# Performance work log

Hardware: AMD Instinct MI355X
Metric: run time of the kernel (lower is better)

The kernel has to match this reference:

```python
import jax, jax.numpy as jnp
import numpy as np

B, T, D = 128, 2048, 4      # batch paths, hedging steps, input features
H, A, W = 64, 32, 10        # hidden_size, attention_dim, memory_length
DMAX = 1.5
SCALE = float(np.sqrt(A))


def setup_inputs() -> dict:
    key = jax.random.key(0)
    ks = jax.random.split(key, 24)

    def rn(k, shape, s=0.1):
        return (jax.random.normal(k, shape) * s).astype(jnp.float32)

    inp = {"x": rn(ks[0], (B, T, D), 1.0)}
    names = [
        ("W_ih0", (4 * H, D)), ("W_hh0", (4 * H, H)), ("b_ih0", (4 * H,)), ("b_hh0", (4 * H,)),
        ("W_ih1", (4 * H, H)), ("W_hh1", (4 * H, H)), ("b_ih1", (4 * H,)), ("b_hh1", (4 * H,)),
        ("Wq", (A, H)), ("bq", (A,)), ("Wk", (A, H)), ("bk", (A,)),
        ("Wv", (H, H)), ("bv", (H,)), ("Wc", (H, 2 * H)), ("bc", (H,)),
        ("Wo1", (H // 2, H)), ("bo1", (H // 2,)), ("Wo2", (1, H // 2)), ("bo2", (1,)),
    ]
    for i, (n, s) in enumerate(names):
        inp[n] = rn(ks[i + 1], s)
    return inp


def _lstm_cell(xt, h, c, Wih, Whh, bih, bhh):
    g = xt @ Wih.T + h @ Whh.T + bih + bhh
    i, f, gg, o = jnp.split(g, 4, axis=-1)  # torch gate order i,f,g,o
    c = jax.nn.sigmoid(f) * c + jax.nn.sigmoid(i) * jnp.tanh(gg)
    h = jax.nn.sigmoid(o) * jnp.tanh(c)
    return h, c


def _forward(x, W_ih0, W_hh0, b_ih0, b_hh0, W_ih1, W_hh1, b_ih1, b_hh1,
             Wq, bq, Wk, bk, Wv, bv, Wc, bc, Wo1, bo1, Wo2, bo2):
    b, t, _ = x.shape
    z = jnp.zeros((b, H), x.dtype)

    def step(carry, xt):
        h0, c0, h1, c1 = carry
        h0, c0 = _lstm_cell(xt, h0, c0, W_ih0, W_hh0, b_ih0, b_hh0)
        h1, c1 = _lstm_cell(h0, h1, c1, W_ih1, W_hh1, b_ih1, b_hh1)
        return (h0, c0, h1, c1), h1

    _, hs = jax.lax.scan(step, (z, z, z, z), jnp.swapaxes(x, 0, 1))  # [T,B,H]
    lstm_out = jnp.swapaxes(hs, 0, 1)  # [B,T,H]

    # sliding-window causal attention over the last W hidden states (strictly past)
    q = lstm_out @ Wq.T + bq          # [B,T,A]
    k = lstm_out @ Wk.T + bk          # [B,T,A]
    v = lstm_out @ Wv.T + bv          # [B,T,H]

    idx = jnp.arange(t)[:, None] - jnp.arange(1, W + 1)[None, :]  # [T,W], t-1..t-W
    mask = idx >= 0
    idxc = jnp.clip(idx, 0, t - 1)
    k_win = k[:, idxc]                # [B,T,W,A]
    v_win = v[:, idxc]                # [B,T,W,H]

    scores = jnp.einsum('bta,btwa->btw', q, k_win) / SCALE
    scores = jnp.where(mask[None], scores, jnp.float32(-1e9))
    weights = jax.nn.softmax(scores, axis=-1)
    context = jnp.einsum('btw,btwh->bth', weights, v_win)  # [B,T,H]

    combined = jnp.concatenate([lstm_out, context], axis=-1) @ Wc.T + bc
    # at t == 0 the original skips attention and uses h_t directly
    combined = jnp.where((jnp.arange(t) == 0)[None, :, None], lstm_out, combined)

    raw = jax.nn.relu(combined @ Wo1.T + bo1) @ Wo2.T + bo2  # [B,T,1]
    return DMAX * jnp.tanh(raw[..., 0])                      # [B,T]


def reference(x, W_ih0, W_hh0, b_ih0, b_hh0, W_ih1, W_hh1, b_ih1, b_hh1,
              Wq, bq, Wk, bk, Wv, bv, Wc, bc, Wo1, bo1, Wo2, bo2):
    return _forward(x, W_ih0, W_hh0, b_ih0, b_hh0, W_ih1, W_hh1, b_ih1, b_hh1,
                    Wq, bq, Wk, bk, Wv, bv, Wc, bc, Wo1, bo1, Wo2, bo2)
```

## Files before the change

### kernel.cpp

```cpp
#include <hip/hip_runtime.h>
#include <hip/hip_bf16.h>
#include <math.h>

#define BB   128
#define TT   2048
#define DD   4
#define HH   64
#define WIN  10
#define TILE 64
#define RWS  (TILE + WIN)

__device__ __forceinline__ float sigf(float x) {
    return __fdividef(1.f, 1.f + __expf(-x));
}
__device__ __forceinline__ float dot4(float4 a, float4 b) {
    return a.x*b.x + a.y*b.y + a.z*b.z + a.w*b.w;
}

#define QB(x, imm) __int_as_float(__builtin_amdgcn_mov_dpp(__float_as_int(x), (imm), 0xF, 0xF, true))
__device__ __forceinline__ float red8(float x) {
    x = x + QB(x, 0xB1);
    x = x + QB(x, 0x4E);
    x = x + QB(x, 0x141);
    return x;
}

__device__ __forceinline__ void act_update(const float gv0, const float gv1,
                                           const float gv2, const float gv3,
                                           const int q, float& c, float& h) {
    float y = gv0;
    y = (q == 1) ? gv1 : y;
    y = (q == 2) ? gv2 : y;
    y = (q == 3) ? gv3 : y;
    y = (q == 2) ? y + y : y;
    float s = sigf(y);
    s = (q == 2) ? s + s - 1.f : s;
    const float ii = QB(s, 0x00);
    const float ff = QB(s, 0x55);
    const float gg = QB(s, 0xAA);
    const float oo = QB(s, 0xFF);
    c = ff * c + ii * gg;
    h = oo * (2.f * sigf(c + c) - 1.f);
}

#define PIN4(v) asm volatile("" : "+v"(v.x), "+v"(v.y), "+v"(v.z), "+v"(v.w))

__global__ __launch_bounds__(512, 1)
void lstm_kernel(const float* __restrict__ x,
                 const float* __restrict__ Wih0, const float* __restrict__ Whh0,
                 const float* __restrict__ bih0, const float* __restrict__ bhh0,
                 const float* __restrict__ Wih1, const float* __restrict__ Whh1,
                 const float* __restrict__ bih1, const float* __restrict__ bhh1,
                 float* __restrict__ lstm_out) {
    __shared__ __align__(16) float h0s[2][HH];
    __shared__ __align__(16) float h1s[2][HH];
    __shared__ __align__(16) float xall[TT * DD];
    __shared__ __align__(16) float hbuf[64 * HH];

    const int tid = threadIdx.x;
    const int u   = tid >> 3;
    const int p   = tid & 7;
    const int q   = tid & 3;
    const int b   = blockIdx.x;

    float4 wh0[4][2], wi1[4][2], wh1[4][2];
    float  wx[4], b0g[4], b1g[4];
#pragma unroll
    for (int g = 0; g < 4; ++g) {
        const int row = g * 64 + u;
        wh0[g][0] = *(const float4*)(Whh0 + row * 64 + 8 * p);
        wh0[g][1] = *(const float4*)(Whh0 + row * 64 + 8 * p + 4);
        wi1[g][0] = *(const float4*)(Wih1 + row * 64 + 8 * p);
        wi1[g][1] = *(const float4*)(Wih1 + row * 64 + 8 * p + 4);
        wh1[g][0] = *(const float4*)(Whh1 + row * 64 + 8 * p);
        wh1[g][1] = *(const float4*)(Whh1 + row * 64 + 8 * p + 4);
        wx[g]  = (p < 4) ? Wih0[row * 4 + p] : 0.f;
        b0g[g] = bih0[row] + bhh0[row];
        b1g[g] = bih1[row] + bhh1[row];
    }
#pragma unroll
    for (int g = 0; g < 4; ++g) {
#pragma unroll
        for (int c = 0; c < 2; ++c) {
            PIN4(wh0[g][c]);
            PIN4(wi1[g][c]);
            PIN4(wh1[g][c]);
        }
        asm volatile("" : "+v"(wx[g]), "+v"(b0g[g]), "+v"(b1g[g]));
    }

    const float* xrow = x + (size_t)b * TT * DD;
    for (int i = tid; i < TT; i += 512)
        *(float4*)(xall + i * 4) = *(const float4*)(xrow + i * 4);
    if (tid < HH) h1s[1][tid] = 0.f;
    float c0 = 0.f, c1 = 0.f;
    __syncthreads();

    {
        const float xa = xall[p & 3];
        float g0v[4];
#pragma unroll
        for (int g = 0; g < 4; ++g) g0v[g] = red8(wx[g] * xa) + b0g[g];
        float h0v;
        act_update(g0v[0], g0v[1], g0v[2], g0v[3], q, c0, h0v);
        if (p == 0) h0s[0][u] = h0v;
    }

    float* orow = lstm_out + (size_t)b * TT * HH;

    for (int t = 0; t < TT; ++t) {
        __syncthreads();
        const float* h0c = h0s[t & 1];
        const float* h1p = h1s[(t + 1) & 1];
        const float4 h0a = *(const float4*)(h0c + 8 * p);
        const float4 h0b = *(const float4*)(h0c + 8 * p + 4);
        const float4 h1a = *(const float4*)(h1p + 8 * p);
        const float4 h1b = *(const float4*)(h1p + 8 * p + 4);

        float g1v[4], g0v[4];
#pragma unroll
        for (int g = 0; g < 4; ++g) {
            const float sA = dot4(wi1[g][0], h0a) + dot4(wh1[g][0], h1a);
            const float sB = dot4(wi1[g][1], h0b) + dot4(wh1[g][1], h1b);
            g1v[g] = sA + sB;
        }
        const float xa = xall[(t + 1 < TT ? t + 1 : t) * 4 + (p & 3)];
#pragma unroll
        for (int g = 0; g < 4; ++g) {
            const float sA = wx[g] * xa + dot4(wh0[g][0], h0a);
            const float sB = dot4(wh0[g][1], h0b);
            g0v[g] = sA + sB;
        }
#pragma unroll
        for (int g = 0; g < 4; ++g) g1v[g] = red8(g1v[g]) + b1g[g];
#pragma unroll
        for (int g = 0; g < 4; ++g) g0v[g] = red8(g0v[g]) + b0g[g];

        {
            float h1vv;
            act_update(g1v[0], g1v[1], g1v[2], g1v[3], q, c1, h1vv);
            if (p == 0) h1s[t & 1][u] = h1vv;
            if (p == 1) hbuf[(t & 63) * HH + u] = h1vv;
        }
        if (t + 1 < TT) {
            float h0vv;
            act_update(g0v[0], g0v[1], g0v[2], g0v[3], q, c0, h0vv);
            if (p == 0) h0s[(t + 1) & 1][u] = h0vv;
        }
        if ((t & 63) == 63) {
            __syncthreads();
            float4*       dst = (float4*)(orow + (size_t)(t - 63) * HH);
            const float4* src = (const float4*)hbuf;
            dst[tid]       = src[tid];
            dst[512 + tid] = src[512 + tid];
        }
    }
}

#define ATTN_LDS_FLOATS 19560

__global__ __launch_bounds__(256, 2)
void attn_kernel(const float* __restrict__ lstm,
                 const float* __restrict__ Wq, const float* __restrict__ bq,
                 const float* __restrict__ Wk, const float* __restrict__ bk,
                 const float* __restrict__ Wv, const float* __restrict__ bv,
                 const float* __restrict__ Wc, const float* __restrict__ bc,
                 const float* __restrict__ Wo1, const float* __restrict__ bo1,
                 const float* __restrict__ Wo2, const float* __restrict__ bo2,
                 float* __restrict__ out) {
    extern __shared__ __align__(16) float lds[];
    float* bias = lds;
    float* ho   = lds + 256;
    float* kb   = lds + 4992;
    float* qb   = lds + 7656;
    float* vb   = lds + 9960;
    float* swr  = lds + 14696;
    float* ctxs = lds + 15464;
    float* cmbs = lds + 4992;
    float* o1s  = lds + 9960;

    const int tid  = threadIdx.x;
    const int b    = blockIdx.x >> 5;
    const int tile = blockIdx.x & 31;
    const int t0   = tile * TILE;

    if (tid < 32) {
        bias[tid]       = bq[tid];
        bias[32 + tid]  = bk[tid];
        bias[192 + tid] = bo1[tid];
        bias[224 + tid] = Wo2[tid];
    }
    if (tid >= 64 && tid < 128) {
        const int j = tid - 64;
        bias[64 + j]  = bv[j];
        bias[128 + j] = bc[j];
    }
    for (int i = tid; i < RWS * 16; i += 256) {
        const int row = i >> 4, c = i & 15;
        const int t = t0 - WIN + row;
        float4 v = make_float4(0.f, 0.f, 0.f, 0.f);
        if (t >= 0) v = *(const float4*)(lstm + ((size_t)b * TT + t) * HH + 4 * c);
        *(float4*)(ho + row * 64 + 4 * c) = v;
    }
    __syncthreads();

    {
        const int h = tid & 63, rq = tid >> 6;
        const int r0 = rq * 19;
        int ri[19];
        float acc[19];
#pragma unroll
        for (int rr = 0; rr < 19; ++rr) { ri[rr] = min(r0 + rr, RWS - 1); acc[rr] = bias[64 + h]; }
#pragma unroll
        for (int k4 = 0; k4 < 16; ++k4) {
            const float4 w = *(const float4*)(Wv + h * 64 + 4 * k4);
#pragma unroll
            for (int rr = 0; rr < 19; ++rr)
                acc[rr] += dot4(w, *(const float4*)(ho + ri[rr] * 64 + 4 * k4));
        }
#pragma unroll
        for (int rr = 0; rr < 19; ++rr) vb[ri[rr] * 64 + h] = acc[rr];
    }
    {
        const int a = tid & 31, rq = tid >> 5;
        const int r0 = rq * 10;
        int ri[10];
        float acc[10];
#pragma unroll
        for (int rr = 0; rr < 10; ++rr) { ri[rr] = min(r0 + rr, RWS - 1); acc[rr] = bias[32 + a]; }
#pragma unroll
        for (int k4 = 0; k4 < 16; ++k4) {
            const float4 w = *(const float4*)(Wk + a * 64 + 4 * k4);
#pragma unroll
            for (int rr = 0; rr < 10; ++rr)
                acc[rr] += dot4(w, *(const float4*)(ho + ri[rr] * 64 + 4 * k4));
        }
#pragma unroll
        for (int rr = 0; rr < 10; ++rr) kb[ri[rr] * 36 + a] = acc[rr];
    }
    {
        const int a = tid & 31, rq = tid >> 5;
        float acc[8];
#pragma unroll
        for (int rr = 0; rr < 8; ++rr) acc[rr] = bias[a];
#pragma unroll
        for (int k4 = 0; k4 < 16; ++k4) {
            const float4 w = *(const float4*)(Wq + a * 64 + 4 * k4);
#pragma unroll
            for (int rr = 0; rr < 8; ++rr)
                acc[rr] += dot4(w, *(const float4*)(ho + (rq * 8 + rr + WIN) * 64 + 4 * k4));
        }
#pragma unroll
        for (int rr = 0; rr < 8; ++rr) qb[(rq * 8 + rr) * 36 + a] = acc[rr];
    }
    __syncthreads();

    for (int i = tid; i < TILE * WIN; i += 256) {
        const int r = i / WIN, l = i - r * WIN;
        const int t = t0 + r;
        float s = -1e30f;
        if (t - 1 - l >= 0) {
            const int kr = r + WIN - 1 - l;
            float acc = 0.f;
#pragma unroll
            for (int a4 = 0; a4 < 8; ++a4)
                acc += dot4(*(const float4*)(qb + r * 36 + 4 * a4),
                            *(const float4*)(kb + kr * 36 + 4 * a4));
            s = acc * 0.17677669529663687f;
        }
        swr[r * 12 + l] = s;
    }
    __syncthreads();
    if (tid < TILE) {
        const int r = tid;
        float sc[WIN], m = -1e30f;
#pragma unroll
        for (int l = 0; l < WIN; ++l) { sc[l] = swr[r * 12 + l]; m = fmaxf(m, sc[l]); }
        float sum = 0.f;
#pragma unroll
        for (int l = 0; l < WIN; ++l) { sc[l] = __expf(sc[l] - m); sum += sc[l]; }
        const float inv = __fdividef(1.f, sum);
#pragma unroll
        for (int l = 0; l < WIN; ++l) swr[r * 12 + l] = sc[l] * inv;
    }
    __syncthreads();
    for (int i = tid; i < TILE * HH; i += 256) {
        const int r = i >> 6, h = i & 63;
        float acc = 0.f;
#pragma unroll
        for (int l = 0; l < WIN; ++l)
            acc += swr[r * 12 + l] * vb[(r + WIN - 1 - l) * 64 + h];
        ctxs[r * 64 + h] = acc;
    }
    __syncthreads();

    {
        const int h = tid & 63, rq = tid >> 6;
        float acc[16];
#pragma unroll
        for (int rr = 0; rr < 16; ++rr) acc[rr] = bias[128 + h];
#pragma unroll
        for (int k4 = 0; k4 < 16; ++k4) {
            const float4 w = *(const float4*)(Wc + h * 128 + 4 * k4);
#pragma unroll
            for (int rr = 0; rr < 16; ++rr)
                acc[rr] += dot4(w, *(const float4*)(ho + (rq * 16 + rr + WIN) * 64 + 4 * k4));
        }
#pragma unroll
        for (int k4 = 0; k4 < 16; ++k4) {
            const float4 w = *(const float4*)(Wc + h * 128 + 64 + 4 * k4);
#pragma unroll
            for (int rr = 0; rr < 16; ++rr)
                acc[rr] += dot4(w, *(const float4*)(ctxs + (rq * 16 + rr) * 64 + 4 * k4));
        }
        if (t0 == 0 && rq == 0) acc[0] = ho[WIN * 64 + h];
#pragma unroll
        for (int rr = 0; rr < 16; ++rr) cmbs[(rq * 16 + rr) * 64 + h] = acc[rr];
    }
    __syncthreads();

    {
        const int m = tid & 31, rq = tid >> 5;
        float acc[8];
#pragma unroll
        for (int rr = 0; rr < 8; ++rr) acc[rr] = bias[192 + m];
#pragma unroll
        for (int k4 = 0; k4 < 16; ++k4) {
            const float4 w = *(const float4*)(Wo1 + m * 64 + 4 * k4);
#pragma unroll
            for (int rr = 0; rr < 8; ++rr)
                acc[rr] += dot4(w, *(const float4*)(cmbs + (rq * 8 + rr) * 64 + 4 * k4));
        }
#pragma unroll
        for (int rr = 0; rr < 8; ++rr)
            o1s[(rq * 8 + rr) * 33 + m] = fmaxf(acc[rr], 0.f);
    }
    __syncthreads();

    if (tid < TILE) {
        const int r = tid;
        float s = bo2[0];
#pragma unroll
        for (int m = 0; m < 32; ++m) s += o1s[r * 33 + m] * bias[224 + m];
        out[(size_t)b * TT + t0 + r] = 1.5f * tanhf(s);
    }
}

extern "C" void kernel_launch(void* const* d_in, const int* in_sizes, int n_in,
                              void* d_out, int out_size, void* d_ws, size_t ws_size,
                              hipStream_t stream) {
    const float* x    = (const float*)d_in[0];
    const float* Wih0 = (const float*)d_in[1];
    const float* Whh0 = (const float*)d_in[2];
    const float* bih0 = (const float*)d_in[3];
    const float* bhh0 = (const float*)d_in[4];
    const float* Wih1 = (const float*)d_in[5];
    const float* Whh1 = (const float*)d_in[6];
    const float* bih1 = (const float*)d_in[7];
    const float* bhh1 = (const float*)d_in[8];
    const float* Wq   = (const float*)d_in[9];
    const float* bq   = (const float*)d_in[10];
    const float* Wk   = (const float*)d_in[11];
    const float* bk   = (const float*)d_in[12];
    const float* Wv   = (const float*)d_in[13];
    const float* bv   = (const float*)d_in[14];
    const float* Wc   = (const float*)d_in[15];
    const float* bc   = (const float*)d_in[16];
    const float* Wo1  = (const float*)d_in[17];
    const float* bo1  = (const float*)d_in[18];
    const float* Wo2  = (const float*)d_in[19];
    const float* bo2  = (const float*)d_in[20];
    float* out = (float*)d_out;

    float* lstm_out = (float*)d_ws;

    lstm_kernel<<<BB, 512, 0, stream>>>(x, Wih0, Whh0, bih0, bhh0,
                                        Wih1, Whh1, bih1, bhh1, lstm_out);

    const int LDS_BYTES = ATTN_LDS_FLOATS * 4;
    hipFuncSetAttribute(reinterpret_cast<const void*>(attn_kernel),
                        hipFuncAttributeMaxDynamicSharedMemorySize, LDS_BYTES);
    attn_kernel<<<BB * (TT / TILE), 256, LDS_BYTES, stream>>>(
        lstm_out, Wq, bq, Wk, bk, Wv, bv, Wc, bc, Wo1, bo1, Wo2, bo2, out);
}
```

Baseline: 2.205 ms.

## Split LSTM layers across dedicated thread groups with 768-thread blocks

The recurrent kernel now uses 768 threads per block. The first 256 threads compute layer-0 gates, with 4 lanes per hidden unit and 16 weights each. The remaining 512 threads compute layer-1 gates, with 8 lanes covering the input and hidden halves. Previously every thread did both layers' dot products serially, so this shortens the per-step critical path by running the two layers in parallel. The cost is more waves per block, and a block-wide barrier that now spans 12 waves every timestep.

```diff
diff --git a/kernel.cpp b/kernel.cpp
--- a/kernel.cpp
+++ b/kernel.cpp
@@ -18,6 +18,11 @@
 }
 
 #define QB(x, imm) __int_as_float(__builtin_amdgcn_mov_dpp(__float_as_int(x), (imm), 0xF, 0xF, true))
+__device__ __forceinline__ float red4(float x) {
+    x = x + QB(x, 0xB1);
+    x = x + QB(x, 0x4E);
+    return x;
+}
 __device__ __forceinline__ float red8(float x) {
     x = x + QB(x, 0xB1);
     x = x + QB(x, 0x4E);
@@ -45,7 +50,7 @@
 
 #define PIN4(v) asm volatile("" : "+v"(v.x), "+v"(v.y), "+v"(v.z), "+v"(v.w))
 
-__global__ __launch_bounds__(512, 1)
+__global__ __launch_bounds__(768, 1) __attribute__((amdgpu_waves_per_eu(3, 3)))
 void lstm_kernel(const float* __restrict__ x,
                  const float* __restrict__ Wih0, const float* __restrict__ Whh0,
                  const float* __restrict__ bih0, const float* __restrict__ bhh0,
@@ -58,51 +63,51 @@
     __shared__ __align__(16) float hbuf[64 * HH];
 
     const int tid = threadIdx.x;
-    const int u   = tid >> 3;
-    const int p   = tid & 7;
-    const int q   = tid & 3;
     const int b   = blockIdx.x;
-
-    float4 wh0[4][2], wi1[4][2], wh1[4][2];
-    float  wx[4], b0g[4], b1g[4];
+    const bool isA = (tid < 256);
+    const int btid = isA ? tid : (tid - 256);
+
+    const int u = isA ? (tid >> 2) : (btid >> 3);
+    const int p = isA ? (tid & 3)  : (btid & 7);
+    const int q = btid & 3;
+
+    float4 wr[4][4];
+    float  wx[4], bg[4];
 #pragma unroll
     for (int g = 0; g < 4; ++g) {
         const int row = g * 64 + u;
-        wh0[g][0] = *(const float4*)(Whh0 + row * 64 + 8 * p);
-        wh0[g][1] = *(const float4*)(Whh0 + row * 64 + 8 * p + 4);
-        wi1[g][0] = *(const float4*)(Wih1 + row * 64 + 8 * p);
-        wi1[g][1] = *(const float4*)(Wih1 + row * 64 + 8 * p + 4);
-        wh1[g][0] = *(const float4*)(Whh1 + row * 64 + 8 * p);
-        wh1[g][1] = *(const float4*)(Whh1 + row * 64 + 8 * p + 4);
-        wx[g]  = (p < 4) ? Wih0[row * 4 + p] : 0.f;
-        b0g[g] = bih0[row] + bhh0[row];
-        b1g[g] = bih1[row] + bhh1[row];
+        const float* src;
+        int col;
+        if (isA) { src = Whh0; col = 16 * p; }
+        else if (p < 4) { src = Wih1; col = 16 * p; }
+        else { src = Whh1; col = 16 * (p - 4); }
+#pragma unroll
+        for (int c = 0; c < 4; ++c)
+            wr[g][c] = *(const float4*)(src + row * 64 + col + 4 * c);
+        wx[g] = (isA && p < 4) ? Wih0[row * 4 + p] : 0.f;
+        bg[g] = isA ? (bih0[row] + bhh0[row]) : (bih1[row] + bhh1[row]);
     }
 #pragma unroll
     for (int g = 0; g < 4; ++g) {
 #pragma unroll
-        for (int c = 0; c < 2; ++c) {
-            PIN4(wh0[g][c]);
-            PIN4(wi1[g][c]);
-            PIN4(wh1[g][c]);
-        }
-        asm volatile("" : "+v"(wx[g]), "+v"(b0g[g]), "+v"(b1g[g]));
+        for (int c = 0; c < 4; ++c) PIN4(wr[g][c]);
+        asm volatile("" : "+v"(wx[g]), "+v"(bg[g]));
     }
 
     const float* xrow = x + (size_t)b * TT * DD;
-    for (int i = tid; i < TT; i += 512)
+    for (int i = tid; i < TT; i += 768)
         *(float4*)(xall + i * 4) = *(const float4*)(xrow + i * 4);
     if (tid < HH) h1s[1][tid] = 0.f;
-    float c0 = 0.f, c1 = 0.f;
-    __syncthreads();
-
-    {
-        const float xa = xall[p & 3];
-        float g0v[4];
-#pragma unroll
-        for (int g = 0; g < 4; ++g) g0v[g] = red8(wx[g] * xa) + b0g[g];
+    float cc = 0.f;
+    __syncthreads();
+
+    if (isA) {
+        const float xa = xall[p];
+        float gv[4];
+#pragma unroll
+        for (int g = 0; g < 4; ++g) gv[g] = red4(wx[g] * xa) + bg[g];
         float h0v;
-        act_update(g0v[0], g0v[1], g0v[2], g0v[3], q, c0, h0v);
+        act_update(gv[0], gv[1], gv[2], gv[3], q, cc, h0v);
         if (p == 0) h0s[0][u] = h0v;
     }
 
@@ -112,47 +117,44 @@
         __syncthreads();
         const float* h0c = h0s[t & 1];
         const float* h1p = h1s[(t + 1) & 1];
-        const float4 h0a = *(const float4*)(h0c + 8 * p);
-        const float4 h0b = *(const float4*)(h0c + 8 * p + 4);
-        const float4 h1a = *(const float4*)(h1p + 8 * p);
-        const float4 h1b = *(const float4*)(h1p + 8 * p + 4);
-
-        float g1v[4], g0v[4];
+
+        const float* hsrc = isA ? h0c : ((p < 4) ? h0c : h1p);
+        const int off = (p & 3) * 16;
+        float4 hv0 = *(const float4*)(hsrc + off);
+        float4 hv1 = *(const float4*)(hsrc + off + 4);
+        float4 hv2 = *(const float4*)(hsrc + off + 8);
+        float4 hv3 = *(const float4*)(hsrc + off + 12);
+
+        const float xa = isA ? xall[(t + 1 < TT ? t + 1 : t) * 4 + p] : 0.f;
+        float gv[4];
 #pragma unroll
         for (int g = 0; g < 4; ++g) {
-            const float sA = dot4(wi1[g][0], h0a) + dot4(wh1[g][0], h1a);
-            const float sB = dot4(wi1[g][1], h0b) + dot4(wh1[g][1], h1b);
-            g1v[g] = sA + sB;
-        }
-        const float xa = xall[(t + 1 < TT ? t + 1 : t) * 4 + (p & 3)];
-#pragma unroll
-        for (int g = 0; g < 4; ++g) {
-            const float sA = wx[g] * xa + dot4(wh0[g][0], h0a);
-            const float sB = dot4(wh0[g][1], h0b);
-            g0v[g] = sA + sB;
-        }
-#pragma unroll
-        for (int g = 0; g < 4; ++g) g1v[g] = red8(g1v[g]) + b1g[g];
-#pragma unroll
-        for (int g = 0; g < 4; ++g) g0v[g] = red8(g0v[g]) + b0g[g];
-
-        {
-            float h1vv;
-            act_update(g1v[0], g1v[1], g1v[2], g1v[3], q, c1, h1vv);
-            if (p == 0) h1s[t & 1][u] = h1vv;
-            if (p == 1) hbuf[(t & 63) * HH + u] = h1vv;
-        }
-        if (t + 1 < TT) {
-            float h0vv;
-            act_update(g0v[0], g0v[1], g0v[2], g0v[3], q, c0, h0vv);
-            if (p == 0) h0s[(t + 1) & 1][u] = h0vv;
-        }
+            const float sA = dot4(wr[g][0], hv0) + dot4(wr[g][1], hv1);
+            const float sB = dot4(wr[g][2], hv2) + dot4(wr[g][3], hv3);
+            gv[g] = wx[g] * xa + sA + sB;
+        }
+        if (isA) {
+#pragma unroll
+            for (int g = 0; g < 4; ++g) gv[g] = red4(gv[g]) + bg[g];
+            if (t + 1 < TT) {
+                float h0v;
+                act_update(gv[0], gv[1], gv[2], gv[3], q, cc, h0v);
+                if (p == 0) h0s[(t + 1) & 1][u] = h0v;
+            }
+        } else {
+#pragma unroll
+            for (int g = 0; g < 4; ++g) gv[g] = red8(gv[g]) + bg[g];
+            float h1v;
+            act_update(gv[0], gv[1], gv[2], gv[3], q, cc, h1v);
+            if (p == 0) h1s[t & 1][u] = h1v;
+            if (p == 1) hbuf[(t & 63) * HH + u] = h1v;
+        }
+
         if ((t & 63) == 63) {
             __syncthreads();
             float4*       dst = (float4*)(orow + (size_t)(t - 63) * HH);
             const float4* src = (const float4*)hbuf;
-            dst[tid]       = src[tid];
-            dst[512 + tid] = src[512 + tid];
+            for (int i = tid; i < 1024; i += 768) dst[i] = src[i];
         }
     }
 }
@@ -374,7 +376,7 @@
 
     float* lstm_out = (float*)d_ws;
 
-    lstm_kernel<<<BB, 512, 0, stream>>>(x, Wih0, Whh0, bih0, bhh0,
+    lstm_kernel<<<BB, 768, 0, stream>>>(x, Wih0, Whh0, bih0, bhh0,
                                         Wih1, Whh1, bih1, bhh1, lstm_out);
 
     const int LDS_BYTES = ATTN_LDS_FLOATS * 4;
```

New measurement: 1.820 ms. 1.21x faster.
